# Kernel optimization log

Hardware: AMD Instinct MI355X
Metric: run time of the kernel (lower is better)

## Reference

```python
import jax, jax.numpy as jnp
import numpy as np

EPS = 1e-6

def setup_inputs() -> dict:
    key = jax.random.key(0)
    M, N, D = 6, 4096, 512
    output = jax.random.normal(key, (M, N, D), dtype=jnp.float32)
    return {"output": output}

def reference(output):
    # output: [M, N, D] stacked per-layer features (already flatten(1)'d)
    M, N, _ = output.shape
    # Gram matrices K_i = X_i @ X_i^T with zeroed diagonal: [M, N, N]
    K = jnp.einsum('ind,imd->inm', output, output)
    K = K * (1.0 - jnp.eye(N, dtype=K.dtype))
    # Double centering H@K@H == K - rowmean - colmean + totalmean
    row = jnp.mean(K, axis=2, keepdims=True)
    col = jnp.mean(K, axis=1, keepdims=True)
    tot = jnp.mean(K, axis=(1, 2), keepdims=True)
    Khat = K - row - col + tot
    # Pairwise HSIC(K_i, K_j) = |sum(Khat_i * Khat_j)| : [M, M]
    S = jnp.abs(jnp.einsum('inm,jnm->ij', Khat, Khat))
    diag = jnp.diagonal(S)
    cka = S / jnp.sqrt(diag[:, None] * diag[None, :] + EPS)
    # Original only fills the strict lower triangle
    hsic_matrix = cka * jnp.tril(jnp.ones((M, M), dtype=cka.dtype), k=-1)
    l = jnp.sum(jnp.abs(hsic_matrix))
    hsic_visual = hsic_matrix + hsic_matrix.T + jnp.eye(M, dtype=cka.dtype)
    return (hsic_visual, l)
```

## Files before the change

### kernel.cpp

```cpp
#include <hip/hip_runtime.h>
#include <hip/hip_bf16.h>
#include <stdint.h>


#define NPTS  4096
#define DF    512
#define ML    6
#define NPAIR 21
#define BKB   128
#define KCHUNK 1024
#define NDIAGBLK 240
#define NOFFBLK  960
#define NGEMMBLK (NDIAGBLK + NOFFBLK)
#define NSTATS   192
#define NTAIL    81
#define TILEB (128 * BKB)

typedef float  f32x4 __attribute__((ext_vector_type(4)));
typedef int    i32x4v __attribute__((ext_vector_type(4)));
typedef int    i32x8v __attribute__((ext_vector_type(8)));
typedef unsigned char u8;

__constant__ int c_PI[NPAIR] = {0,0,0,0,0,0, 1,1,1,1,1, 2,2,2,2, 3,3,3, 4,4, 5};
__constant__ int c_PJ[NPAIR] = {0,1,2,3,4,5, 1,2,3,4,5, 2,3,4,5, 3,4,5, 4,5, 5};
__constant__ int c_DIAGP[ML]  = {0, 6, 11, 15, 18, 20};
__constant__ int c_OFFP[15]   = {1,2,3,4,5, 7,8,9,10, 12,13,14, 16,17, 19};
__constant__ int c_TM[10] = {0,0,0,0, 1,1,1, 2,2, 3};
__constant__ int c_TN[10] = {0,1,2,3, 1,2,3, 2,3, 3};

#define OFF_XT8  0u
#define OFF_CP   12582912u
#define OFF_SP   28311552u
#define OFF_DVP  29097984u
#define OFF_F    29884416u
#define OFF_D    (OFF_F + 1024u)
#define OFF_XS   (OFF_D + 98304u)
#define OFF_DD   (OFF_XS + 98304u)
#define OFF_RD   (OFF_DD + 256u)
#define OFF_T    (OFF_RD + 256u)

#define UNIT_SCALE 127

__device__ __forceinline__ unsigned short f2fp8x2(float a, float b) {
    return (unsigned short)(__builtin_amdgcn_cvt_pk_fp8_f32(a, b, 0, false) & 0xffff);
}

__device__ __forceinline__ void gl2lds16(const void* g, void* l) {
    __builtin_amdgcn_global_load_lds(
        (__attribute__((address_space(1))) void*)g,
        (__attribute__((address_space(3))) void*)l, 16, 0, 0);
}

__device__ __forceinline__ i32x8v frag32(const u8* base, int row, int quad) {
    int sw = row & 7;
    i32x4v lo = *(const i32x4v*)&base[row * BKB + ((2 * quad) ^ sw) * 16];
    i32x4v hi = *(const i32x4v*)&base[row * BKB + ((2 * quad + 1) ^ sw) * 16];
    return __builtin_shufflevector(lo, hi, 0, 1, 2, 3, 4, 5, 6, 7);
}

__device__ __forceinline__ void stage128(const u8* __restrict__ G, u8* L,
                                         int wave, int rl, int g, int k0) {
#pragma unroll
    for (int is = 0; is < 4; ++is) {
        int rbase = is * 32 + wave * 8;
        int r = rbase + rl;
        int gs = g ^ (r & 7);
        gl2lds16(G + (size_t)r * NPTS + k0 + gs * 16, &L[rbase * BKB]);
    }
}

__global__ __launch_bounds__(256) void k_transpose(const float* __restrict__ X,
                                                   u8* __restrict__ Xt8,
                                                   float* __restrict__ sp,
                                                   float* __restrict__ dvp,
                                                   float* __restrict__ F,
                                                   unsigned* __restrict__ cnt,
                                                   float* __restrict__ tbss,
                                                   float* __restrict__ dv,
                                                   float* __restrict__ xs) {
    __shared__ float tT[64][67];
    int nt = blockIdx.x, dt = blockIdx.y, l = blockIdx.z;
    int n0 = nt * 64, d0 = dt * 64;
    int t = threadIdx.x, q = t & 15, r = t >> 4;
    if (dt == 0) {
        int zb = (l << 6) + nt;
        if (t < 64)            dv[zb * 64 + t] = 0.f;
        else if (t < 128)      xs[zb * 64 + (t - 64)] = 0.f;
        if (zb == 0) {
            if (t >= 128 && t < 128 + NPAIR) F[t - 128] = 0.f;
            if (t == 155) *cnt = 0u;
            if (t >= 160 && t < 160 + ML) tbss[t - 160] = 0.f;
        }
    }
    const float4* src = (const float4*)(X + ((size_t)l * NPTS + n0) * DF + d0);
#pragma unroll
    for (int p = 0; p < 4; ++p) {
        int rr = r + 16 * p;
        float4 v = src[(size_t)rr * (DF / 4) + q];
        tT[4 * q + 0][rr] = v.x;
        tT[4 * q + 1][rr] = v.y;
        tT[4 * q + 2][rr] = v.z;
        tT[4 * q + 3][rr] = v.w;
    }
    __syncthreads();
    if (t < 64) {
        float cs = 0.f;
#pragma unroll
        for (int k = 0; k < 64; ++k) {
            int n = (6 * t + k) & 63;
            cs += tT[t][n];
        }
        sp[((l << 6) + nt) * DF + d0 + t] = cs;
    } else if (t < 128) {
        int n = t - 64;
        float rs = 0.f;
#pragma unroll
        for (int d = 0; d < 64; ++d) { float v = tT[d][n]; rs += v * v; }
        dvp[((l << 3) + dt) * NPTS + n0 + n] = rs;
    }
    int dcol = t >> 2, nb = (t & 3) * 16;
    uint4 o;
#pragma unroll
    for (int w2 = 0; w2 < 4; ++w2) {
        int j = nb + w2 * 4;
        unsigned lo = f2fp8x2(tT[dcol][j + 0], tT[dcol][j + 1]);
        unsigned hi = f2fp8x2(tT[dcol][j + 2], tT[dcol][j + 3]);
        ((unsigned*)&o)[w2] = lo | (hi << 16);
    }
    *(uint4*)(Xt8 + ((size_t)(l * DF + d0 + dcol)) * NPTS + n0 + nb) = o;
}

__global__ __launch_bounds__(256, 2) void k_gemm_frob(const u8* __restrict__ Xt8,
                                                      float* __restrict__ CP,
                                                      float* __restrict__ F,
                                                      const float* __restrict__ sp,
                                                      const float* __restrict__ dvp,
                                                      float* __restrict__ dv,
                                                      float* __restrict__ xs,
                                                      float* __restrict__ tbss) {
    __shared__ __align__(16) u8 As[2][TILEB];
    __shared__ __align__(16) u8 Bs[2][TILEB];

    int orig = blockIdx.x;
    int b = (orig < NGEMMBLK) ? (((orig & 7) * (NGEMMBLK >> 3)) + (orig >> 3))
                              : orig;
    int t = threadIdx.x, wave = t >> 6, lane = t & 63;
    int rl = lane >> 3, g = lane & 7;
    int row16 = lane & 15, quad = lane >> 4;

    if (b < NGEMMBLK) {
        const u8* A;
        const u8* B;
        int kLo, li = 0, tt = 0, z, pp = 0;
        bool isDiag = (b < NDIAGBLK);
        if (isDiag) {
            li = b / 40; int rem = b % 40; tt = rem >> 2; z = rem & 3;
            A = Xt8 + ((size_t)(li * DF + c_TM[tt] * 128)) * NPTS;
            B = Xt8 + ((size_t)(li * DF + c_TN[tt] * 128)) * NPTS;
        } else {
            int b2 = b - NDIAGBLK;
            int op = b2 >> 6, rem = b2 & 63;
            int tile = rem >> 2; z = rem & 3;
            pp = c_OFFP[op];
            A = Xt8 + ((size_t)(c_PI[pp] * DF + (tile & 3) * 128)) * NPTS;
            B = Xt8 + ((size_t)(c_PJ[pp] * DF + (tile >> 2) * 128)) * NPTS;
        }
        kLo = z * KCHUNK;

        int wr = (wave >> 1) * 64, wc = (wave & 1) * 64;
        f32x4 acc[4][4];
#pragma unroll
        for (int mi = 0; mi < 4; ++mi)
#pragma unroll
            for (int ni = 0; ni < 4; ++ni) acc[mi][ni] = (f32x4)0.0f;

        stage128(A, As[0], wave, rl, g, kLo);
        stage128(B, Bs[0], wave, rl, g, kLo);
        int cur = 0;
        for (int it = 0; it < KCHUNK / BKB; ++it) {
            if (it < KCHUNK / BKB - 1) {
                int kN = kLo + (it + 1) * BKB;
                stage128(A, As[cur ^ 1], wave, rl, g, kN);
                stage128(B, Bs[cur ^ 1], wave, rl, g, kN);
                asm volatile("s_waitcnt vmcnt(8)" ::: "memory");
            } else {
                asm volatile("s_waitcnt vmcnt(0)" ::: "memory");
            }
            __builtin_amdgcn_s_barrier();
            asm volatile("" ::: "memory");
            i32x8v af[4];
#pragma unroll
            for (int mi = 0; mi < 4; ++mi)
                af[mi] = frag32(As[cur], wr + mi * 16 + row16, quad);
#pragma unroll
            for (int ni = 0; ni < 4; ++ni) {
                i32x8v bf = frag32(Bs[cur], wc + ni * 16 + row16, quad);
#pragma unroll
                for (int mi = 0; mi < 4; ++mi)
                    acc[mi][ni] = __builtin_amdgcn_mfma_scale_f32_16x16x128_f8f6f4(
                        af[mi], bf, acc[mi][ni], 0, 0,
                        0, UNIT_SCALE, 0, UNIT_SCALE);
            }
            asm volatile("s_waitcnt lgkmcnt(0)" ::: "memory");
            __builtin_amdgcn_s_barrier();
            asm volatile("" ::: "memory");
            cur ^= 1;
        }

        if (isDiag) {
            float* cp = CP + (((size_t)(li * 10 + tt) * 4 + z) * 16384) + wave * 4096;
#pragma unroll
            for (int mi = 0; mi < 4; ++mi)
#pragma unroll
                for (int ni = 0; ni < 4; ++ni)
#pragma unroll
                    for (int e = 0; e < 4; ++e)
                        cp[(mi * 4 + ni) * 256 + e * 64 + lane] = acc[mi][ni][e];
        } else {
            float local = 0.f;
#pragma unroll
            for (int mi = 0; mi < 4; ++mi)
#pragma unroll
                for (int ni = 0; ni < 4; ++ni)
#pragma unroll
                    for (int e = 0; e < 4; ++e)
                        local += acc[mi][ni][e] * acc[mi][ni][e];
            for (int off = 32; off; off >>= 1) local += __shfl_down(local, off);
            __shared__ float wsum[4];
            if (lane == 0) wsum[wave] = local;
            __syncthreads();
            if (t == 0) atomicAdd(&F[pp], wsum[0] + wsum[1] + wsum[2] + wsum[3]);
        }
    } else {
        int sid = b - NGEMMBLK;
        int l = sid >> 5, rem = sid & 31, dc = rem >> 2, nc = rem & 3;
        int d0 = dc * 64, n0 = nc * 1024;
        float* scratch = (float*)As;
        float* slp = (float*)As + 256;

        int dl = t & 63, part = t >> 6;
        float a = 0.f;
#pragma unroll 4
        for (int k = 0; k < 16; ++k)
            a += sp[((l << 6) + part * 16 + k) * DF + d0 + dl];
        scratch[t] = a;
        __syncthreads();
        if (t < 64)
            slp[t] = scratch[t] + scratch[64 + t] + scratch[128 + t] + scratch[192 + t];
        __syncthreads();
        if (nc == 0 && t == 0) {
            float q2 = 0.f;
#pragma unroll
            for (int d = 0; d < 64; ++d) q2 += slp[d] * slp[d];
            atomicAdd(&tbss[l], q2);
        }
        int n = n0 + t * 4;
        const u8* xb = Xt8 + (size_t)(l * DF + d0) * NPTS + n;
        float a0 = 0, a1 = 0, a2 = 0, a3 = 0;
#pragma unroll 8
        for (int dd = 0; dd < 64; ++dd) {
            unsigned v = *(const unsigned*)(xb + (size_t)dd * NPTS);
            float sv = slp[dd];
            a0 += sv * __builtin_amdgcn_cvt_f32_fp8(v, 0);
            a1 += sv * __builtin_amdgcn_cvt_f32_fp8(v, 1);
            a2 += sv * __builtin_amdgcn_cvt_f32_fp8(v, 2);
            a3 += sv * __builtin_amdgcn_cvt_f32_fp8(v, 3);
        }
        float* xo = xs + l * NPTS + n;
        atomicAdd(&xo[0], a0); atomicAdd(&xo[1], a1);
        atomicAdd(&xo[2], a2); atomicAdd(&xo[3], a3);
        float4 dp = *(const float4*)(dvp + ((l << 3) + dc) * NPTS + n);
        float* dvo = dv + l * NPTS + n;
        atomicAdd(&dvo[0], dp.x); atomicAdd(&dvo[1], dp.y);
        atomicAdd(&dvo[2], dp.z); atomicAdd(&dvo[3], dp.w);
    }
}

__global__ __launch_bounds__(256) void k_tail(const float* __restrict__ CP,
                                              const float* __restrict__ dv,
                                              const float* __restrict__ xs,
                                              const float* __restrict__ tbss,
                                              float* __restrict__ F,
                                              float* __restrict__ ddot,
                                              float* __restrict__ rdot,
                                              float* __restrict__ tb,
                                              unsigned* __restrict__ cnt,
                                              float* __restrict__ out) {
    __shared__ float wsum[4];
    __shared__ float4 red[256];
    __shared__ int lastFlag;
    __shared__ float tbv[ML];
    __shared__ double hs[ML][ML];
    __shared__ float cka[ML][ML];

    int b = blockIdx.x, t = threadIdx.x;

    if (b < 60) {
        int li = b / 10, tt = b % 10;
        const float* base = CP + (size_t)b * 4 * 16384;
        float a = 0.f;
#pragma unroll 4
        for (int c = 0; c < 64; ++c) {
            int idx = c * 256 + t;
            float v = base[idx] + base[16384 + idx]
                    + base[2 * 16384 + idx] + base[3 * 16384 + idx];
            a += v * v;
        }
        for (int off = 32; off; off >>= 1) a += __shfl_down(a, off);
        if ((t & 63) == 0) wsum[t >> 6] = a;
        __syncthreads();
        if (t == 0) {
            float w = (c_TM[tt] == c_TN[tt]) ? 1.0f : 2.0f;
            atomicAdd(&F[c_DIAGP[li]], w * (wsum[0] + wsum[1] + wsum[2] + wsum[3]));
        }
    } else {
        int p = b - 60, i = c_PI[p], j = c_PJ[p];
        const float invN = 1.0f / (float)NPTS;
        float dd = 0.f, rr = 0.f, sd = 0.f;
        for (int n = t; n < NPTS; n += 256) {
            float di = dv[i * NPTS + n], dj = dv[j * NPTS + n];
            float ri = (xs[i * NPTS + n] - di) * invN;
            float rj = (xs[j * NPTS + n] - dj) * invN;
            dd += di * dj;
            rr += ri * rj;
            sd += di;
        }
        red[t] = make_float4(dd, rr, sd, 0.f);
        __syncthreads();
        for (int h = 128; h > 0; h >>= 1) {
            if (t < h) {
                float4 a = red[t], bb = red[t + h];
                red[t] = make_float4(a.x + bb.x, a.y + bb.y, a.z + bb.z, 0.f);
            }
            __syncthreads();
        }
        if (t == 0) {
            atomicExch(&ddot[p], red[0].x);
            atomicExch(&rdot[p], red[0].y);
            if (i == j)
                atomicExch(&tb[i],
                    (tbss[i] - red[0].z) * (1.0f / ((float)NPTS * (float)NPTS)));
        }
    }

    __syncthreads();
    if (t == 0) {
        __threadfence();
        unsigned old = atomicAdd(cnt, 1u);
        lastFlag = (old == NTAIL - 1);
    }
    __syncthreads();
    if (!lastFlag) return;
    __threadfence();
    if (t < ML) tbv[t] = atomicAdd(&tb[t], 0.0f);
    __syncthreads();
    if (t < NPAIR) {
        int i = c_PI[t], j = c_PJ[t];
        double Fv = (double)atomicAdd(&F[t], 0.0f);
        double dd = (double)atomicAdd(&ddot[t], 0.0f);
        double rd = (double)atomicAdd(&rdot[t], 0.0f);
        double v = Fv - dd - 2.0 * (double)NPTS * rd
                 + (double)NPTS * (double)NPTS * (double)tbv[i] * (double)tbv[j];
        hs[i][j] = v; hs[j][i] = v;
    }
    __syncthreads();
    if (t < ML * ML) {
        int i = t / ML, j = t % ML;
        float v;
        if (i == j) v = 1.0f;
        else v = (float)(fabs(hs[i][j]) / sqrt(hs[i][i] * hs[j][j] + 1e-6));
        cka[i][j] = v;
        out[t] = v;
    }
    __syncthreads();
    if (t == 0) {
        float l = 0.f;
        for (int i = 1; i < ML; ++i)
            for (int j = 0; j < i; ++j) l += cka[i][j];
        out[ML * ML] = l;
    }
}

extern "C" void kernel_launch(void* const* d_in, const int* in_sizes, int n_in,
                              void* d_out, int out_size, void* d_ws, size_t ws_size,
                              hipStream_t stream) {
    (void)in_sizes; (void)n_in; (void)out_size; (void)ws_size;
    const float* X = (const float*)d_in[0];
    float* out = (float*)d_out;
    char* ws = (char*)d_ws;
    u8*    Xt8 = (u8*)(ws + OFF_XT8);
    float* CP  = (float*)(ws + OFF_CP);
    float* sp  = (float*)(ws + OFF_SP);
    float* dvp = (float*)(ws + OFF_DVP);
    float* F   = (float*)(ws + OFF_F);
    unsigned* cnt = (unsigned*)(ws + OFF_F + 256u);
    float* tbss = (float*)(ws + OFF_F + 512u);
    float* dv  = (float*)(ws + OFF_D);
    float* xs  = (float*)(ws + OFF_XS);
    float* dd  = (float*)(ws + OFF_DD);
    float* rd  = (float*)(ws + OFF_RD);
    float* tb  = (float*)(ws + OFF_T);

    hipLaunchKernelGGL(k_transpose, dim3(64, 8, 6), dim3(256), 0, stream,
                       X, Xt8, sp, dvp, F, cnt, tbss, dv, xs);
    hipLaunchKernelGGL(k_gemm_frob, dim3(NGEMMBLK + NSTATS), dim3(256), 0, stream,
                       Xt8, CP, F, sp, dvp, dv, xs, tbss);
    hipLaunchKernelGGL(k_tail, dim3(NTAIL), dim3(256), 0, stream,
                       CP, dv, xs, tbss, F, dd, rd, tb, cnt, out);
}
```

Measured before the change: 129.1 us.

## Drop split-K in Gram GEMM, reduce Frobenius norms directly in-kernel

Removes the 4-way split over the N reduction dimension, so each GEMM block now accumulates the full 4096-long K loop and squares/reduces its own tile into the Frobenius accumulator. The diagonal-pair partial products no longer go to a global scratch buffer to be summed and squared by the tail kernel. This eliminates the partial-tile writes and reads and shrinks the tail kernel to 21 blocks. The XCD block remap is generalized for a block count not divisible by 8. The trade-off is 4x fewer GEMM blocks (300 instead of 1200), each running 4x longer, which lowers parallelism and may leave CUs idle or unbalanced.

Measured after the change: 130.1 us. No clear change (+0.8%).

```diff
diff --git a/kernel.cpp b/kernel.cpp
--- a/kernel.cpp
+++ b/kernel.cpp
@@ -8,12 +8,11 @@
 #define ML    6
 #define NPAIR 21
 #define BKB   128
-#define KCHUNK 1024
-#define NDIAGBLK 240
-#define NOFFBLK  960
+#define NDIAGBLK 60
+#define NOFFBLK  240
 #define NGEMMBLK (NDIAGBLK + NOFFBLK)
 #define NSTATS   192
-#define NTAIL    81
+#define NTAIL    21
 #define TILEB (128 * BKB)
 
 typedef float  f32x4 __attribute__((ext_vector_type(4)));
@@ -29,10 +28,9 @@
 __constant__ int c_TN[10] = {0,1,2,3, 1,2,3, 2,3, 3};
 
 #define OFF_XT8  0u
-#define OFF_CP   12582912u
-#define OFF_SP   28311552u
-#define OFF_DVP  29097984u
-#define OFF_F    29884416u
+#define OFF_SP   12582912u
+#define OFF_DVP  13369344u
+#define OFF_F    14155776u
 #define OFF_D    (OFF_F + 1024u)
 #define OFF_XS   (OFF_D + 98304u)
 #define OFF_DD   (OFF_XS + 98304u)
@@ -131,7 +129,6 @@
 }
 
 __global__ __launch_bounds__(256, 2) void k_gemm_frob(const u8* __restrict__ Xt8,
-                                                      float* __restrict__ CP,
                                                       float* __restrict__ F,
                                                       const float* __restrict__ sp,
                                                       const float* __restrict__ dvp,
@@ -142,8 +139,12 @@
     __shared__ __align__(16) u8 Bs[2][TILEB];
 
     int orig = blockIdx.x;
-    int b = (orig < NGEMMBLK) ? (((orig & 7) * (NGEMMBLK >> 3)) + (orig >> 3))
-                              : orig;
+    int b = orig;
+    if (orig < NGEMMBLK) {
+        int xcd = orig & 7, idx = orig >> 3;
+        const int q = NGEMMBLK >> 3, r = NGEMMBLK & 7;
+        b = (xcd < r ? xcd * (q + 1) : r * (q + 1) + (xcd - r) * q) + idx;
+    }
     int t = threadIdx.x, wave = t >> 6, lane = t & 63;
     int rl = lane >> 3, g = lane & 7;
     int row16 = lane & 15, quad = lane >> 4;
@@ -151,21 +152,20 @@
     if (b < NGEMMBLK) {
         const u8* A;
         const u8* B;
-        int kLo, li = 0, tt = 0, z, pp = 0;
-        bool isDiag = (b < NDIAGBLK);
-        if (isDiag) {
-            li = b / 40; int rem = b % 40; tt = rem >> 2; z = rem & 3;
+        int p;
+        float w = 1.0f;
+        if (b < NDIAGBLK) {
+            int li = b / 10, tt = b % 10;
+            p = c_DIAGP[li];
+            w = (c_TM[tt] == c_TN[tt]) ? 1.0f : 2.0f;
             A = Xt8 + ((size_t)(li * DF + c_TM[tt] * 128)) * NPTS;
             B = Xt8 + ((size_t)(li * DF + c_TN[tt] * 128)) * NPTS;
         } else {
-            int b2 = b - NDIAGBLK;
-            int op = b2 >> 6, rem = b2 & 63;
-            int tile = rem >> 2; z = rem & 3;
-            pp = c_OFFP[op];
-            A = Xt8 + ((size_t)(c_PI[pp] * DF + (tile & 3) * 128)) * NPTS;
-            B = Xt8 + ((size_t)(c_PJ[pp] * DF + (tile >> 2) * 128)) * NPTS;
-        }
-        kLo = z * KCHUNK;
+            int b2 = b - NDIAGBLK, op = b2 >> 4, tile = b2 & 15;
+            p = c_OFFP[op];
+            A = Xt8 + ((size_t)(c_PI[p] * DF + (tile & 3) * 128)) * NPTS;
+            B = Xt8 + ((size_t)(c_PJ[p] * DF + (tile >> 2) * 128)) * NPTS;
+        }
 
         int wr = (wave >> 1) * 64, wc = (wave & 1) * 64;
         f32x4 acc[4][4];
@@ -174,12 +174,13 @@
 #pragma unroll
             for (int ni = 0; ni < 4; ++ni) acc[mi][ni] = (f32x4)0.0f;
 
-        stage128(A, As[0], wave, rl, g, kLo);
-        stage128(B, Bs[0], wave, rl, g, kLo);
+        stage128(A, As[0], wave, rl, g, 0);
+        stage128(B, Bs[0], wave, rl, g, 0);
         int cur = 0;
-        for (int it = 0; it < KCHUNK / BKB; ++it) {
-            if (it < KCHUNK / BKB - 1) {
-                int kN = kLo + (it + 1) * BKB;
+        const int NIT = NPTS / BKB;
+        for (int it = 0; it < NIT; ++it) {
+            if (it < NIT - 1) {
+                int kN = (it + 1) * BKB;
                 stage128(A, As[cur ^ 1], wave, rl, g, kN);
                 stage128(B, Bs[cur ^ 1], wave, rl, g, kN);
                 asm volatile("s_waitcnt vmcnt(8)" ::: "memory");
@@ -207,30 +208,20 @@
             cur ^= 1;
         }
 
-        if (isDiag) {
-            float* cp = CP + (((size_t)(li * 10 + tt) * 4 + z) * 16384) + wave * 4096;
-#pragma unroll
-            for (int mi = 0; mi < 4; ++mi)
-#pragma unroll
-                for (int ni = 0; ni < 4; ++ni)
-#pragma unroll
-                    for (int e = 0; e < 4; ++e)
-                        cp[(mi * 4 + ni) * 256 + e * 64 + lane] = acc[mi][ni][e];
-        } else {
-            float local = 0.f;
-#pragma unroll
-            for (int mi = 0; mi < 4; ++mi)
-#pragma unroll
-                for (int ni = 0; ni < 4; ++ni)
-#pragma unroll
-                    for (int e = 0; e < 4; ++e)
-                        local += acc[mi][ni][e] * acc[mi][ni][e];
-            for (int off = 32; off; off >>= 1) local += __shfl_down(local, off);
-            __shared__ float wsum[4];
-            if (lane == 0) wsum[wave] = local;
-            __syncthreads();
-            if (t == 0) atomicAdd(&F[pp], wsum[0] + wsum[1] + wsum[2] + wsum[3]);
-        }
+        float local = 0.f;
+#pragma unroll
+        for (int mi = 0; mi < 4; ++mi)
+#pragma unroll
+            for (int ni = 0; ni < 4; ++ni)
+#pragma unroll
+                for (int e = 0; e < 4; ++e)
+                    local += acc[mi][ni][e] * acc[mi][ni][e];
+        for (int off = 32; off; off >>= 1) local += __shfl_down(local, off);
+        __shared__ float wsum[4];
+        if (lane == 0) wsum[wave] = local;
+        __syncthreads();
+        if (t == 0)
+            atomicAdd(&F[p], w * (wsum[0] + wsum[1] + wsum[2] + wsum[3]));
     } else {
         int sid = b - NGEMMBLK;
         int l = sid >> 5, rem = sid & 31, dc = rem >> 2, nc = rem & 3;
@@ -276,8 +267,7 @@
     }
 }
 
-__global__ __launch_bounds__(256) void k_tail(const float* __restrict__ CP,
-                                              const float* __restrict__ dv,
+__global__ __launch_bounds__(256) void k_tail(const float* __restrict__ dv,
                                               const float* __restrict__ xs,
                                               const float* __restrict__ tbss,
                                               float* __restrict__ F,
@@ -286,7 +276,6 @@
                                               float* __restrict__ tb,
                                               unsigned* __restrict__ cnt,
                                               float* __restrict__ out) {
-    __shared__ float wsum[4];
     __shared__ float4 red[256];
     __shared__ int lastFlag;
     __shared__ float tbv[ML];
@@ -295,26 +284,8 @@
 
     int b = blockIdx.x, t = threadIdx.x;
 
-    if (b < 60) {
-        int li = b / 10, tt = b % 10;
-        const float* base = CP + (size_t)b * 4 * 16384;
-        float a = 0.f;
-#pragma unroll 4
-        for (int c = 0; c < 64; ++c) {
-            int idx = c * 256 + t;
-            float v = base[idx] + base[16384 + idx]
-                    + base[2 * 16384 + idx] + base[3 * 16384 + idx];
-            a += v * v;
-        }
-        for (int off = 32; off; off >>= 1) a += __shfl_down(a, off);
-        if ((t & 63) == 0) wsum[t >> 6] = a;
-        __syncthreads();
-        if (t == 0) {
-            float w = (c_TM[tt] == c_TN[tt]) ? 1.0f : 2.0f;
-            atomicAdd(&F[c_DIAGP[li]], w * (wsum[0] + wsum[1] + wsum[2] + wsum[3]));
-        }
-    } else {
-        int p = b - 60, i = c_PI[p], j = c_PJ[p];
+    {
+        int p = b, i = c_PI[p], j = c_PJ[p];
         const float invN = 1.0f / (float)NPTS;
         float dd = 0.f, rr = 0.f, sd = 0.f;
         for (int n = t; n < NPTS; n += 256) {
@@ -389,7 +360,6 @@
     float* out = (float*)d_out;
     char* ws = (char*)d_ws;
     u8*    Xt8 = (u8*)(ws + OFF_XT8);
-    float* CP  = (float*)(ws + OFF_CP);
     float* sp  = (float*)(ws + OFF_SP);
     float* dvp = (float*)(ws + OFF_DVP);
     float* F   = (float*)(ws + OFF_F);
@@ -404,7 +374,7 @@
     hipLaunchKernelGGL(k_transpose, dim3(64, 8, 6), dim3(256), 0, stream,
                        X, Xt8, sp, dvp, F, cnt, tbss, dv, xs);
     hipLaunchKernelGGL(k_gemm_frob, dim3(NGEMMBLK + NSTATS), dim3(256), 0, stream,
-                       Xt8, CP, F, sp, dvp, dv, xs, tbss);
+                       Xt8, F, sp, dvp, dv, xs, tbss);
     hipLaunchKernelGGL(k_tail, dim3(NTAIL), dim3(256), 0, stream,
-                       CP, dv, xs, tbss, F, dd, rd, tb, cnt, out);
-}
+                       dv, xs, tbss, F, dd, rd, tb, cnt, out);
+}
```
